# Optimization experiments

Measured on AMD Instinct MI355X. Metric: run time of the kernel, lower is better.

## Reference

```python
import jax, jax.numpy as jnp
import numpy as np

N_NODES = 100000
N_EDGES = 640000
D_IN = 128
D_H = 128


def _lin_params(key, fan_in, fan_out):
    kw, kb = jax.random.split(key)
    s = 1.0 / np.sqrt(fan_in)
    W = jax.random.uniform(kw, (fan_in, fan_out), jnp.float32, -s, s)
    b = jax.random.uniform(kb, (fan_out,), jnp.float32, -s, s)
    return W, b


def setup_inputs() -> dict:
    key = jax.random.key(0)
    ks = jax.random.split(key, 9)
    x = jax.random.normal(ks[0], (N_NODES, D_IN), jnp.float32)
    edge_index = jax.random.randint(ks[1], (2, N_EDGES), 0, N_NODES, dtype=jnp.int64)
    W1, b1 = _lin_params(ks[2], D_IN, D_H)
    W2, b2 = _lin_params(ks[3], D_H, D_H)
    W3, b3 = _lin_params(ks[4], D_H, D_H)
    Wg0, bg0 = _lin_params(ks[5], D_H, D_H)
    Wg1, bg1 = _lin_params(ks[6], D_H, D_H)
    Wo, bo = _lin_params(ks[7], D_H, 1)
    return {"x": x, "edge_index": edge_index,
            "W1": W1, "b1": b1, "W2": W2, "b2": b2, "W3": W3, "b3": b3,
            "Wg0": Wg0, "bg0": bg0, "Wg1": Wg1, "bg1": bg1, "Wo": Wo, "bo": bo}


def gcn_conv(x, src, dst, W, b, n_nodes):
    """PyG GCNConv: D^{-1/2} (A+I) D^{-1/2} X W + b (self-loops added, sym norm)."""
    h = x @ W  # [N, F_out]
    # degree of A+I counted on target side (each self-loop adds 1)
    deg = jnp.zeros((n_nodes,), x.dtype).at[dst].add(1.0) + 1.0
    dis = jax.lax.rsqrt(deg)  # deg^{-1/2}
    coef = dis[src] * dis[dst]  # [E]
    agg = jax.ops.segment_sum(h[src] * coef[:, None], dst, num_segments=n_nodes)
    out = agg + h * (dis * dis)[:, None]  # self-loop term
    return out + b


def reference(x, edge_index, W1, b1, W2, b2, W3, b3, Wg0, bg0, Wg1, bg1, Wo, bo):
    src, dst = edge_index[0], edge_index[1]
    n = x.shape[0]
    lrelu = jax.nn.leaky_relu  # slope 0.01, matches torch default
    # feature extractor MLP
    h = lrelu(x @ W1 + b1)
    h = lrelu(h @ W2 + b2)
    h = lrelu(h @ W3 + b3)
    # input GCN
    h = lrelu(gcn_conv(h, src, dst, Wg0, bg0, n))
    # hidden GCN (dropout is identity in eval mode)
    h = lrelu(gcn_conv(h, src, dst, Wg1, bg1, n))
    # output GCN -> scalar per node
    return gcn_conv(h, src, dst, Wo, bo, n)
```

## Files before the change

kernel.cpp:

```cpp
#include <hip/hip_runtime.h>
#include <hip/hip_bf16.h>

#define D_H 128

typedef __attribute__((ext_vector_type(8))) short bf16x8;
typedef __attribute__((ext_vector_type(4))) float f32x4;

__device__ inline void trunc_split(float x, ushort& hi, ushort& lo) {
    uint u = __builtin_bit_cast(uint, x);
    hi = (ushort)(u >> 16);
    float fh = __builtin_bit_cast(float, u & 0xFFFF0000u);
    float fl = x - fh;
    lo = (ushort)(__builtin_bit_cast(uint, fl) >> 16);
}


__global__ __launch_bounds__(256)
void deg_count_int_kernel(const int* __restrict__ dst, int* __restrict__ cnt, int E) {
    int e = blockIdx.x * 256 + threadIdx.x;
    if (e < E) atomicAdd(&cnt[dst[e]], 1);
}

__global__ __launch_bounds__(256)
void scan_blocks_kernel(const int* __restrict__ cnt, int* __restrict__ rowptr,
                        int* __restrict__ aux, int M) {
    __shared__ int sdata[256];
    const int base = blockIdx.x * 1024 + threadIdx.x * 4;
    int v[4];
#pragma unroll
    for (int i = 0; i < 4; ++i) v[i] = (base + i < M) ? cnt[base + i] : 0;
    int tsum = v[0] + v[1] + v[2] + v[3];
    sdata[threadIdx.x] = tsum;
    __syncthreads();
    int val = tsum;
    for (int off = 1; off < 256; off <<= 1) {
        int n = (threadIdx.x >= off) ? sdata[threadIdx.x - off] : 0;
        __syncthreads();
        val += n;
        sdata[threadIdx.x] = val;
        __syncthreads();
    }
    int run = val - tsum;
#pragma unroll
    for (int i = 0; i < 4; ++i) {
        if (base + i < M) rowptr[base + i] = run;
        run += v[i];
    }
    if (threadIdx.x == 255) aux[blockIdx.x] = val;
}

__global__ __launch_bounds__(128)
void scan_aux_kernel(int* __restrict__ aux, int n) {
    __shared__ int s[128];
    int v = (threadIdx.x < n) ? aux[threadIdx.x] : 0;
    s[threadIdx.x] = v;
    __syncthreads();
    int val = v;
    for (int off = 1; off < 128; off <<= 1) {
        int nn = (threadIdx.x >= off) ? s[threadIdx.x - off] : 0;
        __syncthreads();
        val += nn;
        s[threadIdx.x] = val;
        __syncthreads();
    }
    if (threadIdx.x < n) aux[threadIdx.x] = val - v;
}

__global__ __launch_bounds__(256)
void scan_add_kernel(int* __restrict__ rowptr, int* __restrict__ cursor,
                     const int* __restrict__ aux, const int* __restrict__ cnt,
                     float* __restrict__ dis, int M) {
    int i = blockIdx.x * 256 + threadIdx.x;
    if (i >= M) return;
    int v = rowptr[i] + aux[i >> 10];
    rowptr[i] = v;
    cursor[i] = v;
    dis[i] = rsqrtf((float)cnt[i] + 1.0f);
}

__global__ __launch_bounds__(256)
void scatter_kernel(const int* __restrict__ src, const int* __restrict__ dst,
                    const float* __restrict__ dis, int* __restrict__ cursor,
                    int* __restrict__ es, float* __restrict__ ces, int E) {
    int e = blockIdx.x * 256 + threadIdx.x;
    if (e >= E) return;
    int s = src[e], d = dst[e];
    int pos = atomicAdd(&cursor[d], 1);
    es[pos] = s;
    ces[pos] = dis[s];
}

__global__ __launch_bounds__(256)
void wprep_kernel(const float* __restrict__ W1, const float* __restrict__ W2,
                  const float* __restrict__ W3, const float* __restrict__ W4,
                  const float* __restrict__ W5, ushort* __restrict__ imgs) {
    int w = blockIdx.x >> 6;
    int e = (blockIdx.x & 63) * 256 + threadIdx.x;
    const float* W = w == 0 ? W1 : w == 1 ? W2 : w == 2 ? W3 : w == 3 ? W4 : W5;
    int k = e >> 7, n = e & 127;
    ushort hi, lo;
    trunc_split(W[e], hi, lo);
    ushort* img = imgs + (size_t)w * 34816;
    img[n * 136 + k]         = hi;
    img[17408 + n * 136 + k] = lo;
}

__global__ __launch_bounds__(512, 4)
void fused_mlp4_kernel(const float* __restrict__ X, const ushort* __restrict__ imgs,
                       const float* __restrict__ b1, const float* __restrict__ b2,
                       const float* __restrict__ b3, float* __restrict__ Y, int M) {
    __shared__ ushort sW[34816];
    float* sAct = (float*)sW;

    const int tid  = threadIdx.x;
    const int lane = tid & 63;
    const int wv   = tid >> 6;
    const int bn   = lane & 15;
    const int g    = lane >> 4;
    const int kof  = g * 8;
    const int row0 = blockIdx.x * 128;
    const int lrow = wv * 16 + bn;

    bf16x8 ahi[4], alo[4];
    {
        const int arow = row0 + lrow;
        const bool ok = arow < M;
        const float* ap = X + (size_t)arow * 128 + kof;
#pragma unroll
        for (int kb = 0; kb < 4; ++kb) {
            float f[8];
            if (ok) {
                float4 f0 = *(const float4*)(ap + kb * 32);
                float4 f1 = *(const float4*)(ap + kb * 32 + 4);
                f[0] = f0.x; f[1] = f0.y; f[2] = f0.z; f[3] = f0.w;
                f[4] = f1.x; f[5] = f1.y; f[6] = f1.z; f[7] = f1.w;
            } else {
#pragma unroll
                for (int e = 0; e < 8; ++e) f[e] = 0.f;
            }
            bf16x8 h, l;
#pragma unroll
            for (int e = 0; e < 8; ++e) {
                ushort hb, lb;
                trunc_split(f[e], hb, lb);
                h[e] = (short)hb; l[e] = (short)lb;
            }
            ahi[kb] = h; alo[kb] = l;
        }
    }

    f32x4 acc[8];
    for (int t = 0; t < 4; ++t) {
        {
            const uint4* g4 = (const uint4*)(imgs + (size_t)t * 34816);
            uint4*       s4 = (uint4*)sW;
#pragma unroll
            for (int j = 0; j < 9; ++j) {
                int c = j * 512 + tid;
                if (c < 4352) s4[c] = g4[c];
            }
        }
        __syncthreads();

#pragma unroll
        for (int nt = 0; nt < 8; ++nt) acc[nt] = (f32x4){0.f, 0.f, 0.f, 0.f};
#pragma unroll
        for (int kb = 0; kb < 4; ++kb) {
#pragma unroll
            for (int nt = 0; nt < 8; ++nt) {
                const ushort* ph = &sW[(nt * 16 + bn) * 136 + kb * 32 + kof];
                bf16x8 bh = *(const bf16x8*)ph;
                bf16x8 bl = *(const bf16x8*)(ph + 17408);
                acc[nt] = __builtin_amdgcn_mfma_f32_16x16x32_bf16(ahi[kb], bh, acc[nt], 0, 0, 0);
                acc[nt] = __builtin_amdgcn_mfma_f32_16x16x32_bf16(alo[kb], bh, acc[nt], 0, 0, 0);
                acc[nt] = __builtin_amdgcn_mfma_f32_16x16x32_bf16(ahi[kb], bl, acc[nt], 0, 0, 0);
            }
        }

        if (t < 3) {
            __syncthreads();
            const float* bias = t == 0 ? b1 : t == 1 ? b2 : b3;
#pragma unroll
            for (int nt = 0; nt < 8; ++nt) {
                int col = nt * 16 + bn;
                float bc = bias[col];
#pragma unroll
                for (int i = 0; i < 4; ++i) {
                    float v = acc[nt][i] + bc;
                    v = v > 0.f ? v : 0.01f * v;
                    sAct[(wv * 16 + g * 4 + i) * 132 + col] = v;
                }
            }
#pragma unroll
            for (int kb = 0; kb < 4; ++kb) {
                float4 f0 = *(const float4*)&sAct[lrow * 132 + kb * 32 + kof];
                float4 f1 = *(const float4*)&sAct[lrow * 132 + kb * 32 + kof + 4];
                float f[8] = {f0.x, f0.y, f0.z, f0.w, f1.x, f1.y, f1.z, f1.w};
                bf16x8 h, l;
#pragma unroll
                for (int e = 0; e < 8; ++e) {
                    ushort hb, lb;
                    trunc_split(f[e], hb, lb);
                    h[e] = (short)hb; l[e] = (short)lb;
                }
                ahi[kb] = h; alo[kb] = l;
            }
            __syncthreads();
        } else {
#pragma unroll
            for (int nt = 0; nt < 8; ++nt) {
                int col = nt * 16 + bn;
#pragma unroll
                for (int i = 0; i < 4; ++i) {
                    int row = row0 + wv * 16 + g * 4 + i;
                    if (row < M) Y[(size_t)row * 128 + col] = acc[nt][i];
                }
            }
        }
    }
}

__global__ __launch_bounds__(512, 4)
void gemm_ho_kernel(const float* __restrict__ X, const ushort* __restrict__ img,
                    const float* __restrict__ bias, const float* __restrict__ Wo,
                    float* __restrict__ ho, int M) {
    __shared__ ushort sB[34816];

    const int tid  = threadIdx.x;
    const int lane = tid & 63;
    const int wv   = tid >> 6;
    const int bn   = lane & 15;
    const int g    = lane >> 4;
    const int kof  = g * 8;
    const int row0 = blockIdx.x * 128;
    const int arow = row0 + wv * 16 + bn;

    {
        const uint4* g4 = (const uint4*)img;
        uint4*       s4 = (uint4*)sB;
#pragma unroll
        for (int j = 0; j < 9; ++j) {
            int c = j * 512 + tid;
            if (c < 4352) s4[c] = g4[c];
        }
    }

    bf16x8 ahi[4], alo[4];
    {
        const bool ok = arow < M;
        const float* ap = X + (size_t)arow * 128 + kof;
#pragma unroll
        for (int kb = 0; kb < 4; ++kb) {
            float f[8];
            if (ok) {
                float4 f0 = *(const float4*)(ap + kb * 32);
                float4 f1 = *(const float4*)(ap + kb * 32 + 4);
                f[0] = f0.x; f[1] = f0.y; f[2] = f0.z; f[3] = f0.w;
                f[4] = f1.x; f[5] = f1.y; f[6] = f1.z; f[7] = f1.w;
            } else {
#pragma unroll
                for (int e = 0; e < 8; ++e) f[e] = 0.f;
            }
            bf16x8 h, l;
#pragma unroll
            for (int e = 0; e < 8; ++e) {
                ushort hb, lb;
                trunc_split(f[e], hb, lb);
                h[e] = (short)hb; l[e] = (short)lb;
            }
            ahi[kb] = h; alo[kb] = l;
        }
    }
    __syncthreads();

    f32x4 acc[8];
#pragma unroll
    for (int nt = 0; nt < 8; ++nt) acc[nt] = (f32x4){0.f, 0.f, 0.f, 0.f};
#pragma unroll
    for (int kb = 0; kb < 4; ++kb) {
#pragma unroll
        for (int nt = 0; nt < 8; ++nt) {
            const ushort* ph = &sB[(nt * 16 + bn) * 136 + kb * 32 + kof];
            bf16x8 bh = *(const bf16x8*)ph;
            bf16x8 bl = *(const bf16x8*)(ph + 17408);
            acc[nt] = __builtin_amdgcn_mfma_f32_16x16x32_bf16(ahi[kb], bh, acc[nt], 0, 0, 0);
            acc[nt] = __builtin_amdgcn_mfma_f32_16x16x32_bf16(alo[kb], bh, acc[nt], 0, 0, 0);
            acc[nt] = __builtin_amdgcn_mfma_f32_16x16x32_bf16(ahi[kb], bl, acc[nt], 0, 0, 0);
        }
    }

    float part[4] = {0.f, 0.f, 0.f, 0.f};
#pragma unroll
    for (int nt = 0; nt < 8; ++nt) {
        int col = nt * 16 + bn;
        float bc = bias[col];
        float wo = Wo[col];
#pragma unroll
        for (int i = 0; i < 4; ++i) {
            float v = acc[nt][i] + bc;
            v = v > 0.f ? v : 0.01f * v;
            part[i] += v * wo;
        }
    }
#pragma unroll
    for (int m = 1; m < 16; m <<= 1) {
#pragma unroll
        for (int i = 0; i < 4; ++i) part[i] += __shfl_xor(part[i], m, 64);
    }
    if (bn == 0) {
#pragma unroll
        for (int i = 0; i < 4; ++i) {
            int row = row0 + wv * 16 + g * 4 + i;
            if (row < M) ho[row] = part[i];
        }
    }
}

template<int MODE>
__global__ __launch_bounds__(256)
void gcn_agg_csr_kernel(const float* __restrict__ H, const int* __restrict__ es,
                        const float* __restrict__ ces, const int* __restrict__ rowptr,
                        const int* __restrict__ cnt, const float* __restrict__ dis,
                        const float* __restrict__ bias, float* __restrict__ Y, int M) {
    int w    = (blockIdx.x * 256 + threadIdx.x) >> 6;
    int lane = threadIdx.x & 63;
    if (w >= M) return;

    const float dd  = dis[w];
    const int   beg = rowptr[w];
    const int   n   = cnt[w];

    float2 hv = ((const float2*)H)[(size_t)w * 64 + lane];
    float2 acc;
    acc.x = hv.x * dd * dd;
    acc.y = hv.y * dd * dd;

    int j = 0;
    for (; j + 4 <= n; j += 4) {
        int   s0 = es[beg + j],      s1 = es[beg + j + 1];
        int   s2 = es[beg + j + 2],  s3 = es[beg + j + 3];
        float c0 = ces[beg + j] * dd,     c1 = ces[beg + j + 1] * dd;
        float c2 = ces[beg + j + 2] * dd, c3 = ces[beg + j + 3] * dd;
        float2 v0 = ((const float2*)H)[(size_t)s0 * 64 + lane];
        float2 v1 = ((const float2*)H)[(size_t)s1 * 64 + lane];
        float2 v2 = ((const float2*)H)[(size_t)s2 * 64 + lane];
        float2 v3 = ((const float2*)H)[(size_t)s3 * 64 + lane];
        acc.x += c0 * v0.x + c1 * v1.x + c2 * v2.x + c3 * v3.x;
        acc.y += c0 * v0.y + c1 * v1.y + c2 * v2.y + c3 * v3.y;
    }
    for (; j < n; ++j) {
        int   s = es[beg + j];
        float c = ces[beg + j] * dd;
        float2 v = ((const float2*)H)[(size_t)s * 64 + lane];
        acc.x += c * v.x;
        acc.y += c * v.y;
    }

    if (MODE == 1) {
        float2 bb = ((const float2*)bias)[lane];
        acc.x += bb.x; acc.y += bb.y;
        acc.x = acc.x > 0.f ? acc.x : 0.01f * acc.x;
        acc.y = acc.y > 0.f ? acc.y : 0.01f * acc.y;
    }
    ((float2*)Y)[(size_t)w * 64 + lane] = acc;
}

__global__ __launch_bounds__(256)
void out_csr_kernel(const float* __restrict__ ho, const int* __restrict__ es,
                    const float* __restrict__ ces, const int* __restrict__ rowptr,
                    const int* __restrict__ cnt, const float* __restrict__ dis,
                    const float* __restrict__ bo, float* __restrict__ out, int M) {
    int i = blockIdx.x * 256 + threadIdx.x;
    if (i >= M) return;
    float dd  = dis[i];
    float acc = ho[i] * dd * dd;
    int   beg = rowptr[i], n = cnt[i];
    for (int j = 0; j < n; ++j)
        acc += ces[beg + j] * dd * ho[es[beg + j]];
    out[i] = acc + bo[0];
}


extern "C" void kernel_launch(void* const* d_in, const int* in_sizes, int n_in,
                              void* d_out, int out_size, void* d_ws, size_t ws_size,
                              hipStream_t stream) {
    const float* x   = (const float*)d_in[0];
    const int*   ei  = (const int*)d_in[1];
    const float* W1  = (const float*)d_in[2];
    const float* b1  = (const float*)d_in[3];
    const float* W2  = (const float*)d_in[4];
    const float* b2  = (const float*)d_in[5];
    const float* W3  = (const float*)d_in[6];
    const float* b3  = (const float*)d_in[7];
    const float* Wg0 = (const float*)d_in[8];
    const float* bg0 = (const float*)d_in[9];
    const float* Wg1 = (const float*)d_in[10];
    const float* bg1 = (const float*)d_in[11];
    const float* Wo  = (const float*)d_in[12];
    const float* bo  = (const float*)d_in[13];

    const int M = in_sizes[0] / D_H;
    const int E = in_sizes[1] / 2;
    const int* se = ei;
    const int* de = ei + E;

    float*  A      = (float*)d_ws;
    float*  B      = A + (size_t)M * D_H;
    ushort* Wimg   = (ushort*)(B + (size_t)M * D_H);
    float*  dis    = (float*)(Wimg + 5 * 34816);
    float*  ho     = dis + M;
    float*  ces    = ho + M;
    int*    cnt    = (int*)(ces + E);
    int*    rowptr = cnt + M;
    int*    cursor = rowptr + M;
    int*    es     = cursor + M;
    int*    aux    = es + E;

    float* out = (float*)d_out;

    const int nChunks     = (M + 1023) / 1024;
    const int gemm_blocks = (M + 127) / 128;
    const int node_waves  = (M * 64 + 255) / 256;

    hipMemsetAsync(cnt, 0, M * sizeof(int), stream);
    wprep_kernel<<<320, 256, 0, stream>>>(W1, W2, W3, Wg0, Wg1, Wimg);
    deg_count_int_kernel<<<(E + 255) / 256, 256, 0, stream>>>(de, cnt, E);
    scan_blocks_kernel<<<nChunks, 256, 0, stream>>>(cnt, rowptr, aux, M);
    scan_aux_kernel<<<1, 128, 0, stream>>>(aux, nChunks);
    scan_add_kernel<<<(M + 255) / 256, 256, 0, stream>>>(rowptr, cursor, aux, cnt, dis, M);
    scatter_kernel<<<(E + 255) / 256, 256, 0, stream>>>(se, de, dis, cursor, es, ces, E);

    fused_mlp4_kernel<<<gemm_blocks, 512, 0, stream>>>(x, Wimg, b1, b2, b3, B, M);

    gcn_agg_csr_kernel<1><<<node_waves, 256, 0, stream>>>(B, es, ces, rowptr, cnt, dis, bg0, A, M);

    gcn_agg_csr_kernel<0><<<node_waves, 256, 0, stream>>>(A, es, ces, rowptr, cnt, dis, nullptr, B, M);
    gemm_ho_kernel<<<gemm_blocks, 512, 0, stream>>>(B, Wimg + 4 * 34816, bg1, Wo, ho, M);

    out_csr_kernel<<<(M + 255) / 256, 256, 0, stream>>>(ho, es, ces, rowptr, cnt, dis, bo, out, M);
}
```

Baseline: 291.8 us.

## Switch GEMM kernels to 32x32x16 MFMA tiles with 4-wave blocks

Rewrites the fused MLP and final GCN GEMM kernels to use 32x32x16 bf16 MFMA instead of 16x16x32. Each wave now owns 32 rows instead of 16, and blocks shrink from 8 to 4 waves while still covering 128 rows. The aim is to cut LDS B-fragment reads per MFMA and raise matrix-core utilisation. In exchange, accumulator register pressure rises (64 floats per lane), fewer waves are available to hide latency, and the epilogue's row mapping and cross-lane reduction must change to match.

```diff
diff --git a/kernel.cpp b/kernel.cpp
--- a/kernel.cpp
+++ b/kernel.cpp
@@ -3,8 +3,8 @@
 
 #define D_H 128
 
-typedef __attribute__((ext_vector_type(8))) short bf16x8;
-typedef __attribute__((ext_vector_type(4))) float f32x4;
+typedef __attribute__((ext_vector_type(8)))  short bf16x8;
+typedef __attribute__((ext_vector_type(16))) float f32x16;
 
 __device__ inline void trunc_split(float x, ushort& hi, ushort& lo) {
     uint u = __builtin_bit_cast(uint, x);
@@ -105,33 +105,33 @@
     img[17408 + n * 136 + k] = lo;
 }
 
-__global__ __launch_bounds__(512, 4)
+__global__ __launch_bounds__(256, 2)
 void fused_mlp4_kernel(const float* __restrict__ X, const ushort* __restrict__ imgs,
                        const float* __restrict__ b1, const float* __restrict__ b2,
                        const float* __restrict__ b3, float* __restrict__ Y, int M) {
     __shared__ ushort sW[34816];
     float* sAct = (float*)sW;
 
-    const int tid  = threadIdx.x;
-    const int lane = tid & 63;
-    const int wv   = tid >> 6;
-    const int bn   = lane & 15;
-    const int g    = lane >> 4;
-    const int kof  = g * 8;
-    const int row0 = blockIdx.x * 128;
-    const int lrow = wv * 16 + bn;
-
-    bf16x8 ahi[4], alo[4];
+    const int tid   = threadIdx.x;
+    const int lane  = tid & 63;
+    const int wv    = tid >> 6;
+    const int col32 = lane & 31;
+    const int hl    = lane >> 5;
+    const int kof8  = hl * 8;
+    const int row0  = blockIdx.x * 128;
+    const int lrow  = wv * 32 + col32;
+
+    bf16x8 ahi[8], alo[8];
     {
         const int arow = row0 + lrow;
         const bool ok = arow < M;
-        const float* ap = X + (size_t)arow * 128 + kof;
-#pragma unroll
-        for (int kb = 0; kb < 4; ++kb) {
+        const float* ap = X + (size_t)arow * 128 + kof8;
+#pragma unroll
+        for (int kb = 0; kb < 8; ++kb) {
             float f[8];
             if (ok) {
-                float4 f0 = *(const float4*)(ap + kb * 32);
-                float4 f1 = *(const float4*)(ap + kb * 32 + 4);
+                float4 f0 = *(const float4*)(ap + kb * 16);
+                float4 f1 = *(const float4*)(ap + kb * 16 + 4);
                 f[0] = f0.x; f[1] = f0.y; f[2] = f0.z; f[3] = f0.w;
                 f[4] = f1.x; f[5] = f1.y; f[6] = f1.z; f[7] = f1.w;
             } else {
@@ -149,31 +149,31 @@
         }
     }
 
-    f32x4 acc[8];
+    f32x16 acc[4];
     for (int t = 0; t < 4; ++t) {
         {
             const uint4* g4 = (const uint4*)(imgs + (size_t)t * 34816);
             uint4*       s4 = (uint4*)sW;
 #pragma unroll
-            for (int j = 0; j < 9; ++j) {
-                int c = j * 512 + tid;
-                if (c < 4352) s4[c] = g4[c];
-            }
+            for (int j = 0; j < 17; ++j) s4[j * 256 + tid] = g4[j * 256 + tid];
         }
         __syncthreads();
 
 #pragma unroll
-        for (int nt = 0; nt < 8; ++nt) acc[nt] = (f32x4){0.f, 0.f, 0.f, 0.f};
-#pragma unroll
-        for (int kb = 0; kb < 4; ++kb) {
-#pragma unroll
-            for (int nt = 0; nt < 8; ++nt) {
-                const ushort* ph = &sW[(nt * 16 + bn) * 136 + kb * 32 + kof];
+        for (int nt = 0; nt < 4; ++nt)
+#pragma unroll
+            for (int r = 0; r < 16; ++r) acc[nt][r] = 0.f;
+
+#pragma unroll
+        for (int kb = 0; kb < 8; ++kb) {
+#pragma unroll
+            for (int nt = 0; nt < 4; ++nt) {
+                const ushort* ph = &sW[(nt * 32 + col32) * 136 + kb * 16 + kof8];
                 bf16x8 bh = *(const bf16x8*)ph;
                 bf16x8 bl = *(const bf16x8*)(ph + 17408);
-                acc[nt] = __builtin_amdgcn_mfma_f32_16x16x32_bf16(ahi[kb], bh, acc[nt], 0, 0, 0);
-                acc[nt] = __builtin_amdgcn_mfma_f32_16x16x32_bf16(alo[kb], bh, acc[nt], 0, 0, 0);
-                acc[nt] = __builtin_amdgcn_mfma_f32_16x16x32_bf16(ahi[kb], bl, acc[nt], 0, 0, 0);
+                acc[nt] = __builtin_amdgcn_mfma_f32_32x32x16_bf16(ahi[kb], bh, acc[nt], 0, 0, 0);
+                acc[nt] = __builtin_amdgcn_mfma_f32_32x32x16_bf16(alo[kb], bh, acc[nt], 0, 0, 0);
+                acc[nt] = __builtin_amdgcn_mfma_f32_32x32x16_bf16(ahi[kb], bl, acc[nt], 0, 0, 0);
             }
         }
 
@@ -181,20 +181,21 @@
             __syncthreads();
             const float* bias = t == 0 ? b1 : t == 1 ? b2 : b3;
 #pragma unroll
-            for (int nt = 0; nt < 8; ++nt) {
-                int col = nt * 16 + bn;
+            for (int nt = 0; nt < 4; ++nt) {
+                int col = nt * 32 + col32;
                 float bc = bias[col];
 #pragma unroll
-                for (int i = 0; i < 4; ++i) {
-                    float v = acc[nt][i] + bc;
+                for (int r = 0; r < 16; ++r) {
+                    float v = acc[nt][r] + bc;
                     v = v > 0.f ? v : 0.01f * v;
-                    sAct[(wv * 16 + g * 4 + i) * 132 + col] = v;
+                    int crow = (r & 3) + 8 * (r >> 2) + 4 * hl;
+                    sAct[(wv * 32 + crow) * 132 + col] = v;
                 }
             }
 #pragma unroll
-            for (int kb = 0; kb < 4; ++kb) {
-                float4 f0 = *(const float4*)&sAct[lrow * 132 + kb * 32 + kof];
-                float4 f1 = *(const float4*)&sAct[lrow * 132 + kb * 32 + kof + 4];
+            for (int kb = 0; kb < 8; ++kb) {
+                float4 f0 = *(const float4*)&sAct[lrow * 132 + kb * 16 + kof8];
+                float4 f1 = *(const float4*)&sAct[lrow * 132 + kb * 16 + kof8 + 4];
                 float f[8] = {f0.x, f0.y, f0.z, f0.w, f1.x, f1.y, f1.z, f1.w};
                 bf16x8 h, l;
 #pragma unroll
@@ -208,53 +209,51 @@
             __syncthreads();
         } else {
 #pragma unroll
-            for (int nt = 0; nt < 8; ++nt) {
-                int col = nt * 16 + bn;
-#pragma unroll
-                for (int i = 0; i < 4; ++i) {
-                    int row = row0 + wv * 16 + g * 4 + i;
-                    if (row < M) Y[(size_t)row * 128 + col] = acc[nt][i];
+            for (int nt = 0; nt < 4; ++nt) {
+                int col = nt * 32 + col32;
+#pragma unroll
+                for (int r = 0; r < 16; ++r) {
+                    int row = row0 + wv * 32 + (r & 3) + 8 * (r >> 2) + 4 * hl;
+                    if (row < M) Y[(size_t)row * 128 + col] = acc[nt][r];
                 }
             }
         }
     }
 }
 
-__global__ __launch_bounds__(512, 4)
+__global__ __launch_bounds__(256, 2)
 void gemm_ho_kernel(const float* __restrict__ X, const ushort* __restrict__ img,
                     const float* __restrict__ bias, const float* __restrict__ Wo,
                     float* __restrict__ ho, int M) {
     __shared__ ushort sB[34816];
 
-    const int tid  = threadIdx.x;
-    const int lane = tid & 63;
-    const int wv   = tid >> 6;
-    const int bn   = lane & 15;
-    const int g    = lane >> 4;
-    const int kof  = g * 8;
-    const int row0 = blockIdx.x * 128;
-    const int arow = row0 + wv * 16 + bn;
+    const int tid   = threadIdx.x;
+    const int lane  = tid & 63;
+    const int wv    = tid >> 6;
+    const int col32 = lane & 31;
+    const int hl    = lane >> 5;
+    const int kof8  = hl * 8;
+    const int row0  = blockIdx.x * 128;
+    const int lrow  = wv * 32 + col32;
 
     {
         const uint4* g4 = (const uint4*)img;
         uint4*       s4 = (uint4*)sB;
 #pragma unroll
-        for (int j = 0; j < 9; ++j) {
-            int c = j * 512 + tid;
-            if (c < 4352) s4[c] = g4[c];
-        }
-    }
-
-    bf16x8 ahi[4], alo[4];
+        for (int j = 0; j < 17; ++j) s4[j * 256 + tid] = g4[j * 256 + tid];
+    }
+
+    bf16x8 ahi[8], alo[8];
     {
+        const int arow = row0 + lrow;
         const bool ok = arow < M;
-        const float* ap = X + (size_t)arow * 128 + kof;
-#pragma unroll
-        for (int kb = 0; kb < 4; ++kb) {
+        const float* ap = X + (size_t)arow * 128 + kof8;
+#pragma unroll
+        for (int kb = 0; kb < 8; ++kb) {
             float f[8];
             if (ok) {
-                float4 f0 = *(const float4*)(ap + kb * 32);
-                float4 f1 = *(const float4*)(ap + kb * 32 + 4);
+                float4 f0 = *(const float4*)(ap + kb * 16);
+                float4 f1 = *(const float4*)(ap + kb * 16 + 4);
                 f[0] = f0.x; f[1] = f0.y; f[2] = f0.z; f[3] = f0.w;
                 f[4] = f1.x; f[5] = f1.y; f[6] = f1.z; f[7] = f1.w;
             } else {
@@ -273,45 +272,50 @@
     }
     __syncthreads();
 
-    f32x4 acc[8];
-#pragma unroll
-    for (int nt = 0; nt < 8; ++nt) acc[nt] = (f32x4){0.f, 0.f, 0.f, 0.f};
-#pragma unroll
-    for (int kb = 0; kb < 4; ++kb) {
-#pragma unroll
-        for (int nt = 0; nt < 8; ++nt) {
-            const ushort* ph = &sB[(nt * 16 + bn) * 136 + kb * 32 + kof];
+    f32x16 acc[4];
+#pragma unroll
+    for (int nt = 0; nt < 4; ++nt)
+#pragma unroll
+        for (int r = 0; r < 16; ++r) acc[nt][r] = 0.f;
+
+#pragma unroll
+    for (int kb = 0; kb < 8; ++kb) {
+#pragma unroll
+        for (int nt = 0; nt < 4; ++nt) {
+            const ushort* ph = &sB[(nt * 32 + col32) * 136 + kb * 16 + kof8];
             bf16x8 bh = *(const bf16x8*)ph;
             bf16x8 bl = *(const bf16x8*)(ph + 17408);
-            acc[nt] = __builtin_amdgcn_mfma_f32_16x16x32_bf16(ahi[kb], bh, acc[nt], 0, 0, 0);
-            acc[nt] = __builtin_amdgcn_mfma_f32_16x16x32_bf16(alo[kb], bh, acc[nt], 0, 0, 0);
-            acc[nt] = __builtin_amdgcn_mfma_f32_16x16x32_bf16(ahi[kb], bl, acc[nt], 0, 0, 0);
-        }
-    }
-
-    float part[4] = {0.f, 0.f, 0.f, 0.f};
-#pragma unroll
-    for (int nt = 0; nt < 8; ++nt) {
-        int col = nt * 16 + bn;
+            acc[nt] = __builtin_amdgcn_mfma_f32_32x32x16_bf16(ahi[kb], bh, acc[nt], 0, 0, 0);
+            acc[nt] = __builtin_amdgcn_mfma_f32_32x32x16_bf16(alo[kb], bh, acc[nt], 0, 0, 0);
+            acc[nt] = __builtin_amdgcn_mfma_f32_32x32x16_bf16(ahi[kb], bl, acc[nt], 0, 0, 0);
+        }
+    }
+
+    float part[16];
+#pragma unroll
+    for (int r = 0; r < 16; ++r) part[r] = 0.f;
+#pragma unroll
+    for (int nt = 0; nt < 4; ++nt) {
+        int col = nt * 32 + col32;
         float bc = bias[col];
         float wo = Wo[col];
 #pragma unroll
-        for (int i = 0; i < 4; ++i) {
-            float v = acc[nt][i] + bc;
+        for (int r = 0; r < 16; ++r) {
+            float v = acc[nt][r] + bc;
             v = v > 0.f ? v : 0.01f * v;
-            part[i] += v * wo;
-        }
-    }
-#pragma unroll
-    for (int m = 1; m < 16; m <<= 1) {
-#pragma unroll
-        for (int i = 0; i < 4; ++i) part[i] += __shfl_xor(part[i], m, 64);
-    }
-    if (bn == 0) {
-#pragma unroll
-        for (int i = 0; i < 4; ++i) {
-            int row = row0 + wv * 16 + g * 4 + i;
-            if (row < M) ho[row] = part[i];
+            part[r] += v * wo;
+        }
+    }
+#pragma unroll
+    for (int m = 1; m < 32; m <<= 1) {
+#pragma unroll
+        for (int r = 0; r < 16; ++r) part[r] += __shfl_xor(part[r], m, 64);
+    }
+    if (col32 == 0) {
+#pragma unroll
+        for (int r = 0; r < 16; ++r) {
+            int row = row0 + wv * 32 + (r & 3) + 8 * (r >> 2) + 4 * hl;
+            if (row < M) ho[row] = part[r];
         }
     }
 }
@@ -430,12 +434,12 @@
     scan_add_kernel<<<(M + 255) / 256, 256, 0, stream>>>(rowptr, cursor, aux, cnt, dis, M);
     scatter_kernel<<<(E + 255) / 256, 256, 0, stream>>>(se, de, dis, cursor, es, ces, E);
 
-    fused_mlp4_kernel<<<gemm_blocks, 512, 0, stream>>>(x, Wimg, b1, b2, b3, B, M);
+    fused_mlp4_kernel<<<gemm_blocks, 256, 0, stream>>>(x, Wimg, b1, b2, b3, B, M);
 
     gcn_agg_csr_kernel<1><<<node_waves, 256, 0, stream>>>(B, es, ces, rowptr, cnt, dis, bg0, A, M);
 
     gcn_agg_csr_kernel<0><<<node_waves, 256, 0, stream>>>(A, es, ces, rowptr, cnt, dis, nullptr, B, M);
-    gemm_ho_kernel<<<gemm_blocks, 512, 0, stream>>>(B, Wimg + 4 * 34816, bg1, Wo, ho, M);
+    gemm_ho_kernel<<<gemm_blocks, 256, 0, stream>>>(B, Wimg + 4 * 34816, bg1, Wo, ho, M);
 
     out_csr_kernel<<<(M + 255) / 256, 256, 0, stream>>>(ho, es, ces, rowptr, cnt, dis, bo, out, M);
 }
```

Measured after the change: 295.4 us. No clear change (+1.2%).
